# Performance work log

Measured on AMD Instinct MI355X. Metric: run time of the kernel, lower is better.

Reference implementation:

```python
import jax, jax.numpy as jnp
import numpy as np

N_NODES = 100000
N_EDGES = 1600000
N_GRAPHS = 64
D_IN = 3
HIDDEN = 256
N_CLASSES = 10
NEG_SLOPE = 0.01  # torch F.leaky_relu default


def gcn_conv(x, W, b, src, dst, n_nodes):
    """GCNConv: D^{-1/2}(A+I)D^{-1/2} X W + b with self-loops."""
    h = x @ W  # [N, H]
    ones = jnp.ones(src.shape[0], h.dtype)
    deg = jax.ops.segment_sum(ones, dst, num_segments=n_nodes) + 1.0  # +1 self-loop
    dinv = jax.lax.rsqrt(deg)
    coef = dinv[src] * dinv[dst]  # [E]
    agg = jax.ops.segment_sum(h[src] * coef[:, None], dst, num_segments=n_nodes)
    agg = agg + h * (1.0 / deg)[:, None]  # self-loop contribution (norm = 1/deg)
    return agg + b


def leaky_relu(v):
    return jnp.where(v >= 0, v, NEG_SLOPE * v)


def setup_inputs() -> dict:
    key = jax.random.key(0)
    ks = jax.random.split(key, 12)
    x = jax.random.normal(ks[0], (N_NODES, D_IN), dtype=jnp.float32)
    edge_index = jax.random.randint(ks[1], (2, N_EDGES), 0, N_NODES, dtype=jnp.int32)
    batch = jnp.sort(jax.random.randint(ks[2], (N_NODES,), 0, N_GRAPHS, dtype=jnp.int32))
    s1 = 1.0 / np.sqrt(D_IN)
    s2 = 1.0 / np.sqrt(HIDDEN)
    W1 = jax.random.uniform(ks[3], (D_IN, HIDDEN), jnp.float32, -s1, s1)
    b1 = jnp.zeros((HIDDEN,), jnp.float32)
    W2 = jax.random.uniform(ks[4], (HIDDEN, HIDDEN), jnp.float32, -s2, s2)
    b2 = jnp.zeros((HIDDEN,), jnp.float32)
    W3 = jax.random.uniform(ks[5], (HIDDEN, HIDDEN), jnp.float32, -s2, s2)
    b3 = jnp.zeros((HIDDEN,), jnp.float32)
    Wc = jax.random.uniform(ks[6], (HIDDEN, N_CLASSES), jnp.float32, -s2, s2)
    bc = jax.random.uniform(ks[7], (N_CLASSES,), jnp.float32, -s2, s2)
    return {"x": x, "edge_index": edge_index, "batch": batch,
            "W1": W1, "b1": b1, "W2": W2, "b2": b2, "W3": W3, "b3": b3,
            "Wc": Wc, "bc": bc}


def reference(x, edge_index, batch, W1, b1, W2, b2, W3, b3, Wc, bc):
    src, dst = edge_index[0], edge_index[1]
    h = leaky_relu(gcn_conv(x, W1, b1, src, dst, N_NODES))
    h = leaky_relu(gcn_conv(h, W2, b2, src, dst, N_NODES))
    h = leaky_relu(gcn_conv(h, W3, b3, src, dst, N_NODES))
    # global mean pool over graphs
    sums = jax.ops.segment_sum(h, batch, num_segments=N_GRAPHS)
    cnt = jax.ops.segment_sum(jnp.ones((N_NODES,), h.dtype), batch, num_segments=N_GRAPHS)
    pooled = sums / jnp.maximum(cnt, 1.0)[:, None]  # [G, H]
    logits = pooled @ Wc + bc
    return jax.nn.softmax(logits, axis=1)
```

## Files before the change

### kernel.cpp

```cpp
#include <hip/hip_runtime.h>
#include <hip/hip_bf16.h>
#include <hip/hip_fp16.h>
#include <cstdint>
#include <cstddef>

#define N_NODES   100000
#define N_EDGES   1600000
#define N_GRAPHS  64
#define HIDDEN    256
#define N_CLASSES 10
#define NEG_SLOPE 0.01f

#define E_PAD    (N_EDGES + 8 * N_NODES)
#define GEMM_BLOCKS 391

#define PART_EDGES  8192
#define PART_BLOCKS ((N_EDGES + PART_EDGES - 1) / PART_EDGES)
#define SUB_BITS 10
#define SUB_SIZE 1024
#define N_SUB    ((N_NODES + SUB_SIZE - 1) / SUB_SIZE)
#define CAP_SUB  17408

typedef __attribute__((ext_vector_type(4))) float f32x4;
typedef __attribute__((ext_vector_type(2))) float f32x2;

__device__ __forceinline__ float bf2f(unsigned short u) {
    return __uint_as_float(((unsigned int)u) << 16);
}

__device__ __forceinline__ unsigned char f2fp8(float v) {
    return (unsigned char)(__builtin_amdgcn_cvt_pk_fp8_f32(v, v, 0, false) & 0xff);
}

__device__ __forceinline__ unsigned int rec_pack(int s, float c) {
    __half h = __float2half(c);
    unsigned short hb = reinterpret_cast<const __half_raw*>(&h)->x;
    return ((unsigned int)hb << 17) | (unsigned int)s;
}
__device__ __forceinline__ float rec_coef(unsigned int u) {
    __half_raw hr; hr.x = (unsigned short)(u >> 17);
    return __half2float(*reinterpret_cast<const __half*>(&hr));
}

__global__ __launch_bounds__(256) void k_partition(const int* __restrict__ src, const int* __restrict__ dst,
                                                   int* __restrict__ gcur, unsigned int* __restrict__ bucket) {
    __shared__ int lcnt[N_SUB];
    __shared__ int lbase[N_SUB];
    __shared__ int gbase[N_SUB];
    __shared__ unsigned int stage[PART_EDGES];
    int tid = threadIdx.x;
    for (int i = tid; i < N_SUB; i += 256) lcnt[i] = 0;
    __syncthreads();
    int e0 = blockIdx.x * PART_EDGES + tid * 8;
    for (int g = 0; g < 4; ++g) {
        int e = e0 + g * 2048;
        if (e < N_EDGES) {
            int4 da = *(const int4*)(dst + e);
            int4 db = *(const int4*)(dst + e + 4);
            int d[8] = {da.x, da.y, da.z, da.w, db.x, db.y, db.z, db.w};
#pragma unroll
            for (int j = 0; j < 8; ++j) atomicAdd(&lcnt[d[j] >> SUB_BITS], 1);
        }
    }
    __syncthreads();
    if (tid == 0) {
        int s = 0;
        for (int r = 0; r < N_SUB; ++r) { lbase[r] = s; s += lcnt[r]; }
    }
    __syncthreads();
    for (int i = tid; i < N_SUB; i += 256) {
        gbase[i] = atomicAdd(&gcur[i * 16], lcnt[i]);
        lcnt[i] = lbase[i];
    }
    __syncthreads();
    for (int g = 0; g < 4; ++g) {
        int e = e0 + g * 2048;
        if (e < N_EDGES) {
            int4 da = *(const int4*)(dst + e);
            int4 db = *(const int4*)(dst + e + 4);
            int4 sa = *(const int4*)(src + e);
            int4 sb = *(const int4*)(src + e + 4);
            int d[8] = {da.x, da.y, da.z, da.w, db.x, db.y, db.z, db.w};
            int s[8] = {sa.x, sa.y, sa.z, sa.w, sb.x, sb.y, sb.z, sb.w};
#pragma unroll
            for (int j = 0; j < 8; ++j) {
                int r = d[j] >> SUB_BITS;
                int p = atomicAdd(&lcnt[r], 1);
                stage[p] = ((unsigned int)(d[j] & (SUB_SIZE - 1)) << 17) | (unsigned int)s[j];
            }
        }
    }
    __syncthreads();
    int wv = tid >> 6, ln = tid & 63;
    for (int r = wv; r < N_SUB; r += 4) {
        int base = lbase[r], n = lcnt[r] - base, gb = gbase[r];
        unsigned int* dp = bucket + (size_t)r * CAP_SUB + gb;
        for (int k = ln; k < n; k += 64) dp[k] = stage[base + k];
    }
}

__global__ __launch_bounds__(512) void k_hist3(const unsigned int* __restrict__ bucket,
                                               const int* __restrict__ gcur, int* __restrict__ cnt) {
    int sub = blockIdx.x;
    __shared__ int hist[SUB_SIZE];
    for (int i = threadIdx.x; i < SUB_SIZE; i += 512) hist[i] = 0;
    __syncthreads();
    int n = gcur[sub * 16];
    const unsigned int* bp = bucket + (size_t)sub * CAP_SUB;
    for (int i0 = threadIdx.x * 8; i0 < n; i0 += 512 * 8) {
        uint4 ua = *(const uint4*)(bp + i0);
        uint4 ub = *(const uint4*)(bp + i0 + 4);
        unsigned int u[8] = {ua.x, ua.y, ua.z, ua.w, ub.x, ub.y, ub.z, ub.w};
        int m = n - i0; if (m > 8) m = 8;
#pragma unroll
        for (int j = 0; j < 8; ++j) if (j < m) atomicAdd(&hist[u[j] >> 17], 1);
    }
    __syncthreads();
    int base = sub * SUB_SIZE;
    for (int i = threadIdx.x; i < SUB_SIZE; i += 512)
        if (base + i < N_NODES) cnt[base + i] = hist[i];
}

__global__ __launch_bounds__(512) void k_fill3(const unsigned int* __restrict__ bucket,
                                               const int* __restrict__ gcur,
                                               const float* __restrict__ dinv,
                                               const int* __restrict__ off,
                                               unsigned int* __restrict__ rec) {
    int sub = blockIdx.x;
    __shared__ int lcur[SUB_SIZE];
    __shared__ float ldv[SUB_SIZE];
    int nb0 = sub * SUB_SIZE;
    for (int i = threadIdx.x; i < SUB_SIZE; i += 512) {
        int node = nb0 + i;
        lcur[i] = (node < N_NODES) ? off[node] : 0;
        ldv[i]  = (node < N_NODES) ? dinv[node] : 0.f;
    }
    __syncthreads();
    int n = gcur[sub * 16];
    const unsigned int* bp = bucket + (size_t)sub * CAP_SUB;
    for (int i0 = threadIdx.x * 8; i0 < n; i0 += 512 * 8) {
        uint4 ua = *(const uint4*)(bp + i0);
        uint4 ub = *(const uint4*)(bp + i0 + 4);
        unsigned int u[8] = {ua.x, ua.y, ua.z, ua.w, ub.x, ub.y, ub.z, ub.w};
        int m = n - i0; if (m > 8) m = 8;
        float ds[8];
#pragma unroll
        for (int j = 0; j < 8; ++j) {
            int s = (j < m) ? (int)(u[j] & 0x1ffff) : 0;
            ds[j] = dinv[s];
        }
#pragma unroll
        for (int j = 0; j < 8; ++j) {
            if (j < m) {
                int dr = (int)(u[j] >> 17);
                float c = ds[j] * ldv[dr];
                int p = atomicAdd(&lcur[dr], 1);
                rec[p] = rec_pack((int)(u[j] & 0x1ffff), c);
            }
        }
    }
}

__global__ void k_graph_bounds(const int* __restrict__ batch,
                               int* __restrict__ gstart, int* __restrict__ gcnt) {
    int g = threadIdx.x;
    int lo = 0, hi = N_NODES;
    while (lo < hi) { int mid = (lo + hi) >> 1; if (batch[mid] < g) lo = mid + 1; else hi = mid; }
    __shared__ int sh[N_GRAPHS + 1];
    sh[g] = lo;
    if (g == 0) sh[N_GRAPHS] = N_NODES;
    __syncthreads();
    gstart[g] = sh[g];
    gcnt[g]   = sh[g + 1] - sh[g];
}

__global__ void k_dinv_xpad(const int* __restrict__ cnt, const float* __restrict__ x,
                            float* __restrict__ dinv, float4* __restrict__ xp) {
    int i = blockIdx.x * 256 + threadIdx.x;
    if (i < N_NODES) {
        dinv[i] = rsqrtf((float)cnt[i] + 1.0f);
        xp[i] = make_float4(x[i * 3 + 0], x[i * 3 + 1], x[i * 3 + 2], 0.f);
    }
}

__global__ void k_scanA(const int* __restrict__ cnt, int* __restrict__ out, int* __restrict__ bsum) {
    __shared__ int sh[256];
    int tid = threadIdx.x;
    int base = blockIdx.x * 1024 + tid * 4;
    int v[4]; int s = 0;
#pragma unroll
    for (int i = 0; i < 4; i++) {
        int idx = base + i;
        v[i] = (idx < N_NODES) ? ((cnt[idx] + 7) & ~7) : 0;
        s += v[i];
    }
    sh[tid] = s; __syncthreads();
    for (int off = 1; off < 256; off <<= 1) {
        int t = (tid >= off) ? sh[tid - off] : 0;
        __syncthreads();
        sh[tid] += t;
        __syncthreads();
    }
    int excl = sh[tid] - s;
    if (tid == 255) bsum[blockIdx.x] = sh[255];
#pragma unroll
    for (int i = 0; i < 4; i++) { int idx = base + i; if (idx < N_NODES) out[idx] = excl; excl += v[i]; }
}

__global__ void k_scanB(int* __restrict__ bsum, int nb) {
    __shared__ int sh[128];
    int tid = threadIdx.x;
    int v = (tid < nb) ? bsum[tid] : 0;
    sh[tid] = v; __syncthreads();
    for (int off = 1; off < 128; off <<= 1) {
        int t = (tid >= off) ? sh[tid - off] : 0;
        __syncthreads();
        sh[tid] += t;
        __syncthreads();
    }
    if (tid < nb) bsum[tid] = sh[tid] - v;
}

__global__ void k_scanC(int* __restrict__ off_arr, const int* __restrict__ bsum,
                        const int* __restrict__ cnt, unsigned int* __restrict__ rec) {
    int i = blockIdx.x * 256 + threadIdx.x;
    if (i < N_NODES) {
        int v = off_arr[i] + bsum[i >> 10];
        off_arr[i] = v;
        int c  = cnt[i];
        int cp = (c + 7) & ~7;
        for (int p = v + c; p < v + cp; ++p) rec[p] = 0u;
        if (i == N_NODES - 1) off_arr[N_NODES] = v + cp;
    }
}

__global__ void k_wprep(const float* __restrict__ W, unsigned char* __restrict__ Wswz) {
    int n = blockIdx.x; int k = threadIdx.x;
    unsigned char v = f2fp8(W[k * HIDDEN + n]);
    int k0 = k >> 5, nt = n >> 4;
    int lane = (((k >> 3) & 3) << 4) | (n & 15);
    int j = k & 7;
    Wswz[(size_t)(((k0 * 16) + nt) * 64 + lane) * 8 + j] = v;
}

__global__ void k_agg3(const float4* __restrict__ xp, const int* __restrict__ off,
                       const unsigned int* __restrict__ rec, const float* __restrict__ dinv,
                       float4* __restrict__ ax) {
    int i = blockIdx.x * 256 + threadIdx.x;
    if (i >= N_NODES) return;
    float di = dinv[i];
    float selfc = di * di;
    float4 xi = xp[i];
    float a0 = xi.x * selfc, a1 = xi.y * selfc, a2 = xi.z * selfc;
    int e = off[i], e1 = off[i + 1];
    for (; e < e1; e += 4) {
        uint4 rr = *(const uint4*)(rec + e);
        int s0 = rr.x & 0x1ffff, s1 = rr.y & 0x1ffff, s2 = rr.z & 0x1ffff, s3 = rr.w & 0x1ffff;
        float c0 = rec_coef(rr.x), c1 = rec_coef(rr.y), c2 = rec_coef(rr.z), c3 = rec_coef(rr.w);
        float4 x0 = xp[s0], x1 = xp[s1], x2 = xp[s2], x3 = xp[s3];
        a0 += c0 * x0.x + c1 * x1.x + c2 * x2.x + c3 * x3.x;
        a1 += c0 * x0.y + c1 * x1.y + c2 * x2.y + c3 * x3.y;
        a2 += c0 * x0.z + c1 * x1.z + c2 * x2.z + c3 * x3.z;
    }
    ax[i] = make_float4(a0, a1, a2, 0.f);
}

__global__ void k_l1(const float4* __restrict__ ax, const float* __restrict__ W1,
                     const float* __restrict__ b1, unsigned char* __restrict__ out) {
    int node = blockIdx.x; int c = threadIdx.x;
    float4 a = ax[node];
    float v = a.x * W1[c] + a.y * W1[HIDDEN + c] + a.z * W1[2 * HIDDEN + c] + b1[c];
    v = v >= 0.f ? v : NEG_SLOPE * v;
    out[(size_t)node * HIDDEN + c] = f2fp8(v);
}

__global__ __launch_bounds__(512, 2) void k_gemm_mfma(const unsigned char* __restrict__ A,
                                                      const unsigned char* __restrict__ Wswz,
                                                      unsigned char* __restrict__ C, int M) {
    __shared__ long Bs[8192];
    __shared__ unsigned int St[8][320];
    int tid = threadIdx.x;
    {
        const float4* gsrc = (const float4*)Wswz;
        float4* ldst = (float4*)Bs;
#pragma unroll
        for (int i = 0; i < 8; ++i) ldst[tid + 512 * i] = gsrc[tid + 512 * i];
    }
    __syncthreads();
    int lane = tid & 63, wv = tid >> 6;
    int quad = lane >> 4, r = lane & 15;
    int nstrips = M >> 4;
    unsigned int* stw = &St[wv][0];
    int rrow = lane >> 2, rseg = lane & 3;
    for (int s = blockIdx.x * 8 + wv; s < nstrips; s += GEMM_BLOCKS * 8) {
        int m0 = s * 16;
        const long* Ab = (const long*)(A + (size_t)(m0 + r) * HIDDEN) + quad;
        long af[8];
#pragma unroll
        for (int k0 = 0; k0 < 8; ++k0) af[k0] = Ab[k0 * 4];
        f32x4 acc[16];
#pragma unroll
        for (int i = 0; i < 16; i++) acc[i] = (f32x4){0.f, 0.f, 0.f, 0.f};
#pragma unroll
        for (int k0 = 0; k0 < 8; ++k0) {
#pragma unroll
            for (int nt = 0; nt < 16; ++nt) {
                long w = Bs[(k0 * 16 + nt) * 64 + lane];
                acc[nt] = __builtin_amdgcn_mfma_f32_16x16x32_fp8_fp8(w, af[k0], acc[nt], 0, 0, 0);
            }
        }
#pragma unroll
        for (int q4 = 0; q4 < 4; ++q4) {
#pragma unroll
            for (int t = 0; t < 4; ++t) {
                f32x4 a = acc[q4 * 4 + t];
                unsigned int pk = __builtin_amdgcn_cvt_pk_fp8_f32(a[0], a[1], 0, false);
                pk = __builtin_amdgcn_cvt_pk_fp8_f32(a[2], a[3], pk, true);
                stw[r * 20 + t * 4 + quad] = pk;
            }
            uint4 v = *(const uint4*)&stw[rrow * 20 + rseg * 4];
            *(uint4*)(C + (size_t)(m0 + rrow) * HIDDEN + q4 * 64 + rseg * 16) = v;
        }
    }
}

__global__ __launch_bounds__(256) void k_agg(const unsigned char* __restrict__ h,
                                             const float* __restrict__ bias,
                                             const int* __restrict__ off, const unsigned int* __restrict__ rec,
                                             const float* __restrict__ dinv,
                                             unsigned char* __restrict__ out) {
    int node = (blockIdx.x * 256 + threadIdx.x) >> 6;
    int lane = threadIdx.x & 63;
    if (node >= N_NODES) return;
    float di = dinv[node];
    float selfc = di * di;
    unsigned int hv = *(const unsigned int*)(h + (size_t)node * HIDDEN + lane * 4);
    f32x2 hlo = __builtin_amdgcn_cvt_pk_f32_fp8(hv, false);
    f32x2 hhi = __builtin_amdgcn_cvt_pk_f32_fp8(hv, true);
    float4 bv = ((const float4*)bias)[lane];
    float4 acc = make_float4(bv.x + hlo.x * selfc, bv.y + hlo.y * selfc,
                             bv.z + hhi.x * selfc, bv.w + hhi.y * selfc);
    int e = off[node], e1 = off[node + 1];
    for (; e < e1; e += 8) {
        uint4 ra = *(const uint4*)(rec + e);
        uint4 rb = *(const uint4*)(rec + e + 4);
        unsigned int w0 = *(const unsigned int*)(h + (size_t)(ra.x & 0x1ffff) * HIDDEN + lane * 4);
        unsigned int w1 = *(const unsigned int*)(h + (size_t)(ra.y & 0x1ffff) * HIDDEN + lane * 4);
        unsigned int w2 = *(const unsigned int*)(h + (size_t)(ra.z & 0x1ffff) * HIDDEN + lane * 4);
        unsigned int w3 = *(const unsigned int*)(h + (size_t)(ra.w & 0x1ffff) * HIDDEN + lane * 4);
        unsigned int w4 = *(const unsigned int*)(h + (size_t)(rb.x & 0x1ffff) * HIDDEN + lane * 4);
        unsigned int w5 = *(const unsigned int*)(h + (size_t)(rb.y & 0x1ffff) * HIDDEN + lane * 4);
        unsigned int w6 = *(const unsigned int*)(h + (size_t)(rb.z & 0x1ffff) * HIDDEN + lane * 4);
        unsigned int w7 = *(const unsigned int*)(h + (size_t)(rb.w & 0x1ffff) * HIDDEN + lane * 4);
        float c0 = rec_coef(ra.x), c1 = rec_coef(ra.y), c2 = rec_coef(ra.z), c3 = rec_coef(ra.w);
        float c4 = rec_coef(rb.x), c5 = rec_coef(rb.y), c6 = rec_coef(rb.z), c7 = rec_coef(rb.w);
        f32x2 l0 = __builtin_amdgcn_cvt_pk_f32_fp8(w0, false), g0 = __builtin_amdgcn_cvt_pk_f32_fp8(w0, true);
        f32x2 l1 = __builtin_amdgcn_cvt_pk_f32_fp8(w1, false), g1 = __builtin_amdgcn_cvt_pk_f32_fp8(w1, true);
        f32x2 l2 = __builtin_amdgcn_cvt_pk_f32_fp8(w2, false), g2 = __builtin_amdgcn_cvt_pk_f32_fp8(w2, true);
        f32x2 l3 = __builtin_amdgcn_cvt_pk_f32_fp8(w3, false), g3 = __builtin_amdgcn_cvt_pk_f32_fp8(w3, true);
        f32x2 l4 = __builtin_amdgcn_cvt_pk_f32_fp8(w4, false), g4 = __builtin_amdgcn_cvt_pk_f32_fp8(w4, true);
        f32x2 l5 = __builtin_amdgcn_cvt_pk_f32_fp8(w5, false), g5 = __builtin_amdgcn_cvt_pk_f32_fp8(w5, true);
        f32x2 l6 = __builtin_amdgcn_cvt_pk_f32_fp8(w6, false), g6 = __builtin_amdgcn_cvt_pk_f32_fp8(w6, true);
        f32x2 l7 = __builtin_amdgcn_cvt_pk_f32_fp8(w7, false), g7 = __builtin_amdgcn_cvt_pk_f32_fp8(w7, true);
        acc.x += c0 * l0.x + c1 * l1.x + c2 * l2.x + c3 * l3.x
               + c4 * l4.x + c5 * l5.x + c6 * l6.x + c7 * l7.x;
        acc.y += c0 * l0.y + c1 * l1.y + c2 * l2.y + c3 * l3.y
               + c4 * l4.y + c5 * l5.y + c6 * l6.y + c7 * l7.y;
        acc.z += c0 * g0.x + c1 * g1.x + c2 * g2.x + c3 * g3.x
               + c4 * g4.x + c5 * g5.x + c6 * g6.x + c7 * g7.x;
        acc.w += c0 * g0.y + c1 * g1.y + c2 * g2.y + c3 * g3.y
               + c4 * g4.y + c5 * g5.y + c6 * g6.y + c7 * g7.y;
    }
    acc.x = acc.x >= 0.f ? acc.x : NEG_SLOPE * acc.x;
    acc.y = acc.y >= 0.f ? acc.y : NEG_SLOPE * acc.y;
    acc.z = acc.z >= 0.f ? acc.z : NEG_SLOPE * acc.z;
    acc.w = acc.w >= 0.f ? acc.w : NEG_SLOPE * acc.w;
    unsigned int pk = __builtin_amdgcn_cvt_pk_fp8_f32(acc.x, acc.y, 0, false);
    pk = __builtin_amdgcn_cvt_pk_fp8_f32(acc.z, acc.w, pk, true);
    *(unsigned int*)(out + (size_t)node * HIDDEN + lane * 4) = pk;
}

__global__ void k_pool(const unsigned char* __restrict__ h, const int* __restrict__ gstart,
                       const int* __restrict__ gcnt, float* __restrict__ pooled) {
    int g = blockIdx.x, chunk = blockIdx.y, t = threadIdx.x;
    int s = gstart[g], c = gcnt[g];
    int i0 = s + (int)(((long long)c * chunk) / 16);
    int i1 = s + (int)(((long long)c * (chunk + 1)) / 16);
    float acc = 0.f;
    for (int i = i0; i < i1; ++i) {
        f32x2 v = __builtin_amdgcn_cvt_pk_f32_fp8((unsigned int)h[(size_t)i * HIDDEN + t], false);
        acc += v.x;
    }
    atomicAdd(&pooled[g * HIDDEN + t], acc);
}

__global__ void k_head(const float* __restrict__ pooled, const int* __restrict__ gcnt,
                       const float* __restrict__ Wc, const float* __restrict__ bc,
                       float* __restrict__ out) {
    int g = blockIdx.x; int l = threadIdx.x;
    float inv = 1.0f / fmaxf((float)gcnt[g], 1.0f);
    float p[4];
#pragma unroll
    for (int i = 0; i < 4; i++) p[i] = pooled[g * HIDDEN + l + i * 64] * inv;
    __shared__ float logits[N_CLASSES];
#pragma unroll
    for (int j = 0; j < N_CLASSES; j++) {
        float s = 0.f;
#pragma unroll
        for (int i = 0; i < 4; i++) s += p[i] * Wc[(l + i * 64) * N_CLASSES + j];
        for (int o = 32; o > 0; o >>= 1) s += __shfl_down(s, o, 64);
        if (l == 0) logits[j] = s + bc[j];
    }
    __syncthreads();
    if (l == 0) {
        float m = logits[0];
        for (int j = 1; j < N_CLASSES; j++) m = fmaxf(m, logits[j]);
        float e[N_CLASSES]; float sum = 0.f;
        for (int j = 0; j < N_CLASSES; j++) { e[j] = expf(logits[j] - m); sum += e[j]; }
        for (int j = 0; j < N_CLASSES; j++) out[g * N_CLASSES + j] = e[j] / sum;
    }
}

extern "C" void kernel_launch(void* const* d_in, const int* in_sizes, int n_in,
                              void* d_out, int out_size, void* d_ws, size_t ws_size,
                              hipStream_t stream) {
    const float* x     = (const float*)d_in[0];
    const int*   edge  = (const int*)d_in[1];
    const int*   batch = (const int*)d_in[2];
    const float* W1 = (const float*)d_in[3];
    const float* b1 = (const float*)d_in[4];
    const float* W2 = (const float*)d_in[5];
    const float* b2 = (const float*)d_in[6];
    const float* W3 = (const float*)d_in[7];
    const float* b3 = (const float*)d_in[8];
    const float* Wc = (const float*)d_in[9];
    const float* bc = (const float*)d_in[10];
    float* out = (float*)d_out;
    const int* srcp = edge;
    const int* dstp = edge + N_EDGES;

    char* ws = (char*)d_ws;
    size_t off = 0;
    auto alloc = [&](size_t bytes) -> char* {
        char* p = ws + off;
        off += (bytes + 255) & ~(size_t)255;
        return p;
    };
    unsigned char* hA   = (unsigned char*)alloc((size_t)N_NODES * HIDDEN);
    unsigned char* hB   = (unsigned char*)alloc((size_t)N_NODES * HIDDEN);
    unsigned char* Wz2  = (unsigned char*)alloc((size_t)HIDDEN * HIDDEN);
    unsigned char* Wz3  = (unsigned char*)alloc((size_t)HIDDEN * HIDDEN);
    int*   deg_cnt  = (int*)alloc((size_t)N_NODES * 4);
    float* dinv     = (float*)alloc((size_t)N_NODES * 4);
    int*   csr_off  = (int*)alloc((size_t)(N_NODES + 1) * 4);
    unsigned int* csr_rec = (unsigned int*)alloc((size_t)E_PAD * 4);
    float4* ax      = (float4*)alloc((size_t)N_NODES * 16);
    float4* xp      = (float4*)alloc((size_t)N_NODES * 16);
    int*   gcnt     = (int*)alloc((size_t)N_GRAPHS * 4);
    int*   gstart   = (int*)alloc((size_t)N_GRAPHS * 4);
    float* pooled   = (float*)alloc((size_t)N_GRAPHS * HIDDEN * 4);
    int*   bsum     = (int*)alloc(128 * 4);
    int*   gcur     = (int*)alloc((size_t)N_SUB * 16 * 4);

    unsigned int* bucket = (unsigned int*)hB;

    hipMemsetAsync(gcur, 0, (size_t)N_SUB * 16 * 4, stream);
    hipMemsetAsync(pooled, 0, (size_t)N_GRAPHS * HIDDEN * 4, stream);

    int nb  = (N_NODES + 255) / 256;
    int sblocks = (N_NODES + 1023) / 1024;

    k_partition<<<PART_BLOCKS, 256, 0, stream>>>(srcp, dstp, gcur, bucket);
    k_graph_bounds<<<1, 64, 0, stream>>>(batch, gstart, gcnt);
    k_hist3<<<N_SUB, 512, 0, stream>>>(bucket, gcur, deg_cnt);
    k_dinv_xpad<<<nb, 256, 0, stream>>>(deg_cnt, x, dinv, xp);
    k_scanA<<<sblocks, 256, 0, stream>>>(deg_cnt, csr_off, bsum);
    k_scanB<<<1, 128, 0, stream>>>(bsum, sblocks);
    k_scanC<<<nb, 256, 0, stream>>>(csr_off, bsum, deg_cnt, csr_rec);
    k_fill3<<<N_SUB, 512, 0, stream>>>(bucket, gcur, dinv, csr_off, csr_rec);
    k_wprep<<<HIDDEN, HIDDEN, 0, stream>>>(W2, Wz2);
    k_wprep<<<HIDDEN, HIDDEN, 0, stream>>>(W3, Wz3);

    k_agg3<<<nb, 256, 0, stream>>>(xp, csr_off, csr_rec, dinv, ax);
    k_l1<<<N_NODES, 256, 0, stream>>>(ax, W1, b1, hA);

    int aggb = (N_NODES + 3) / 4;
    k_gemm_mfma<<<GEMM_BLOCKS, 512, 0, stream>>>(hA, Wz2, hB, N_NODES);
    k_agg<<<aggb, 256, 0, stream>>>(hB, b2, csr_off, csr_rec, dinv, hA);
    k_gemm_mfma<<<GEMM_BLOCKS, 512, 0, stream>>>(hA, Wz3, hB, N_NODES);
    k_agg<<<aggb, 256, 0, stream>>>(hB, b3, csr_off, csr_rec, dinv, hA);
    dim3 pg(N_GRAPHS, 16);
    k_pool<<<pg, 256, 0, stream>>>(hA, gstart, gcnt, pooled);
    k_head<<<N_GRAPHS, 64, 0, stream>>>(pooled, gcnt, Wc, bc, out);
}
```

Measured before the change: 455.7 us.

## Fuse dinv/xpad into hist, batch layer-1 nodes per block, column-slice aggregation

Folds the dinv and padded-x computation into the degree histogram kernel, which removes one launch and one re-read of the counts. Layer-1 projection now handles 32 nodes per block with W1 and b1 cached in shared memory, instead of one block per node. The aggregation kernel now assigns 8 threads per node, each covering a 32-column slice, and spreads the 8 slices across consecutive blocks. The intent is to cut per-node gather traffic per block and improve cache locality, at the cost of re-reading the CSR records 8 times.

After: 702.1 us. 54.1% more time.

```diff
diff --git a/kernel.cpp b/kernel.cpp
--- a/kernel.cpp
+++ b/kernel.cpp
@@ -100,7 +100,9 @@
 }
 
 __global__ __launch_bounds__(512) void k_hist3(const unsigned int* __restrict__ bucket,
-                                               const int* __restrict__ gcur, int* __restrict__ cnt) {
+                                               const int* __restrict__ gcur, int* __restrict__ cnt,
+                                               const float* __restrict__ x,
+                                               float* __restrict__ dinv, float4* __restrict__ xp) {
     int sub = blockIdx.x;
     __shared__ int hist[SUB_SIZE];
     for (int i = threadIdx.x; i < SUB_SIZE; i += 512) hist[i] = 0;
@@ -117,8 +119,15 @@
     }
     __syncthreads();
     int base = sub * SUB_SIZE;
-    for (int i = threadIdx.x; i < SUB_SIZE; i += 512)
-        if (base + i < N_NODES) cnt[base + i] = hist[i];
+    for (int i = threadIdx.x; i < SUB_SIZE; i += 512) {
+        int node = base + i;
+        if (node < N_NODES) {
+            int c = hist[i];
+            cnt[node] = c;
+            dinv[node] = rsqrtf((float)c + 1.0f);
+            xp[node] = make_float4(x[node * 3 + 0], x[node * 3 + 1], x[node * 3 + 2], 0.f);
+        }
+    }
 }
 
 __global__ __launch_bounds__(512) void k_fill3(const unsigned int* __restrict__ bucket,
@@ -172,15 +181,6 @@
     __syncthreads();
     gstart[g] = sh[g];
     gcnt[g]   = sh[g + 1] - sh[g];
-}
-
-__global__ void k_dinv_xpad(const int* __restrict__ cnt, const float* __restrict__ x,
-                            float* __restrict__ dinv, float4* __restrict__ xp) {
-    int i = blockIdx.x * 256 + threadIdx.x;
-    if (i < N_NODES) {
-        dinv[i] = rsqrtf((float)cnt[i] + 1.0f);
-        xp[i] = make_float4(x[i * 3 + 0], x[i * 3 + 1], x[i * 3 + 2], 0.f);
-    }
 }
 
 __global__ void k_scanA(const int* __restrict__ cnt, int* __restrict__ out, int* __restrict__ bsum) {
@@ -265,13 +265,22 @@
     ax[i] = make_float4(a0, a1, a2, 0.f);
 }
 
-__global__ void k_l1(const float4* __restrict__ ax, const float* __restrict__ W1,
-                     const float* __restrict__ b1, unsigned char* __restrict__ out) {
-    int node = blockIdx.x; int c = threadIdx.x;
-    float4 a = ax[node];
-    float v = a.x * W1[c] + a.y * W1[HIDDEN + c] + a.z * W1[2 * HIDDEN + c] + b1[c];
-    v = v >= 0.f ? v : NEG_SLOPE * v;
-    out[(size_t)node * HIDDEN + c] = f2fp8(v);
+__global__ __launch_bounds__(256) void k_l1(const float4* __restrict__ ax, const float* __restrict__ W1,
+                                            const float* __restrict__ b1, unsigned char* __restrict__ out) {
+    __shared__ float w0s[HIDDEN], w1s[HIDDEN], w2s[HIDDEN], bbs[HIDDEN];
+    int t = threadIdx.x;
+    w0s[t] = W1[t]; w1s[t] = W1[HIDDEN + t]; w2s[t] = W1[2 * HIDDEN + t]; bbs[t] = b1[t];
+    __syncthreads();
+    int base = blockIdx.x * 32;
+#pragma unroll 4
+    for (int i = 0; i < 32; ++i) {
+        int node = base + i;
+        if (node >= N_NODES) break;
+        float4 a = ax[node];
+        float v = a.x * w0s[t] + a.y * w1s[t] + a.z * w2s[t] + bbs[t];
+        v = v >= 0.f ? v : NEG_SLOPE * v;
+        out[(size_t)node * HIDDEN + t] = f2fp8(v);
+    }
 }
 
 __global__ __launch_bounds__(512, 2) void k_gemm_mfma(const unsigned char* __restrict__ A,
@@ -329,29 +338,31 @@
                                              const int* __restrict__ off, const unsigned int* __restrict__ rec,
                                              const float* __restrict__ dinv,
                                              unsigned char* __restrict__ out) {
-    int node = (blockIdx.x * 256 + threadIdx.x) >> 6;
-    int lane = threadIdx.x & 63;
+    int slice = blockIdx.x & 7;
+    int node = (blockIdx.x >> 3) * 32 + (threadIdx.x >> 3);
+    int sl = threadIdx.x & 7;
     if (node >= N_NODES) return;
+    int coloff = slice * 32 + sl * 4;
     float di = dinv[node];
     float selfc = di * di;
-    unsigned int hv = *(const unsigned int*)(h + (size_t)node * HIDDEN + lane * 4);
+    unsigned int hv = *(const unsigned int*)(h + (size_t)node * HIDDEN + coloff);
     f32x2 hlo = __builtin_amdgcn_cvt_pk_f32_fp8(hv, false);
     f32x2 hhi = __builtin_amdgcn_cvt_pk_f32_fp8(hv, true);
-    float4 bv = ((const float4*)bias)[lane];
-    float4 acc = make_float4(bv.x + hlo.x * selfc, bv.y + hlo.y * selfc,
-                             bv.z + hhi.x * selfc, bv.w + hhi.y * selfc);
+    float4 bv = *(const float4*)(bias + coloff);
+    float a0 = bv.x + hlo.x * selfc, a1 = bv.y + hlo.y * selfc;
+    float a2 = bv.z + hhi.x * selfc, a3 = bv.w + hhi.y * selfc;
     int e = off[node], e1 = off[node + 1];
     for (; e < e1; e += 8) {
         uint4 ra = *(const uint4*)(rec + e);
         uint4 rb = *(const uint4*)(rec + e + 4);
-        unsigned int w0 = *(const unsigned int*)(h + (size_t)(ra.x & 0x1ffff) * HIDDEN + lane * 4);
-        unsigned int w1 = *(const unsigned int*)(h + (size_t)(ra.y & 0x1ffff) * HIDDEN + lane * 4);
-        unsigned int w2 = *(const unsigned int*)(h + (size_t)(ra.z & 0x1ffff) * HIDDEN + lane * 4);
-        unsigned int w3 = *(const unsigned int*)(h + (size_t)(ra.w & 0x1ffff) * HIDDEN + lane * 4);
-        unsigned int w4 = *(const unsigned int*)(h + (size_t)(rb.x & 0x1ffff) * HIDDEN + lane * 4);
-        unsigned int w5 = *(const unsigned int*)(h + (size_t)(rb.y & 0x1ffff) * HIDDEN + lane * 4);
-        unsigned int w6 = *(const unsigned int*)(h + (size_t)(rb.z & 0x1ffff) * HIDDEN + lane * 4);
-        unsigned int w7 = *(const unsigned int*)(h + (size_t)(rb.w & 0x1ffff) * HIDDEN + lane * 4);
+        unsigned int w0 = *(const unsigned int*)(h + (size_t)(ra.x & 0x1ffff) * HIDDEN + coloff);
+        unsigned int w1 = *(const unsigned int*)(h + (size_t)(ra.y & 0x1ffff) * HIDDEN + coloff);
+        unsigned int w2 = *(const unsigned int*)(h + (size_t)(ra.z & 0x1ffff) * HIDDEN + coloff);
+        unsigned int w3 = *(const unsigned int*)(h + (size_t)(ra.w & 0x1ffff) * HIDDEN + coloff);
+        unsigned int w4 = *(const unsigned int*)(h + (size_t)(rb.x & 0x1ffff) * HIDDEN + coloff);
+        unsigned int w5 = *(const unsigned int*)(h + (size_t)(rb.y & 0x1ffff) * HIDDEN + coloff);
+        unsigned int w6 = *(const unsigned int*)(h + (size_t)(rb.z & 0x1ffff) * HIDDEN + coloff);
+        unsigned int w7 = *(const unsigned int*)(h + (size_t)(rb.w & 0x1ffff) * HIDDEN + coloff);
         float c0 = rec_coef(ra.x), c1 = rec_coef(ra.y), c2 = rec_coef(ra.z), c3 = rec_coef(ra.w);
         float c4 = rec_coef(rb.x), c5 = rec_coef(rb.y), c6 = rec_coef(rb.z), c7 = rec_coef(rb.w);
         f32x2 l0 = __builtin_amdgcn_cvt_pk_f32_fp8(w0, false), g0 = __builtin_amdgcn_cvt_pk_f32_fp8(w0, true);
@@ -362,22 +373,22 @@
         f32x2 l5 = __builtin_amdgcn_cvt_pk_f32_fp8(w5, false), g5 = __builtin_amdgcn_cvt_pk_f32_fp8(w5, true);
         f32x2 l6 = __builtin_amdgcn_cvt_pk_f32_fp8(w6, false), g6 = __builtin_amdgcn_cvt_pk_f32_fp8(w6, true);
         f32x2 l7 = __builtin_amdgcn_cvt_pk_f32_fp8(w7, false), g7 = __builtin_amdgcn_cvt_pk_f32_fp8(w7, true);
-        acc.x += c0 * l0.x + c1 * l1.x + c2 * l2.x + c3 * l3.x
-               + c4 * l4.x + c5 * l5.x + c6 * l6.x + c7 * l7.x;
-        acc.y += c0 * l0.y + c1 * l1.y + c2 * l2.y + c3 * l3.y
-               + c4 * l4.y + c5 * l5.y + c6 * l6.y + c7 * l7.y;
-        acc.z += c0 * g0.x + c1 * g1.x + c2 * g2.x + c3 * g3.x
-               + c4 * g4.x + c5 * g5.x + c6 * g6.x + c7 * g7.x;
-        acc.w += c0 * g0.y + c1 * g1.y + c2 * g2.y + c3 * g3.y
-               + c4 * g4.y + c5 * g5.y + c6 * g6.y + c7 * g7.y;
-    }
-    acc.x = acc.x >= 0.f ? acc.x : NEG_SLOPE * acc.x;
-    acc.y = acc.y >= 0.f ? acc.y : NEG_SLOPE * acc.y;
-    acc.z = acc.z >= 0.f ? acc.z : NEG_SLOPE * acc.z;
-    acc.w = acc.w >= 0.f ? acc.w : NEG_SLOPE * acc.w;
-    unsigned int pk = __builtin_amdgcn_cvt_pk_fp8_f32(acc.x, acc.y, 0, false);
-    pk = __builtin_amdgcn_cvt_pk_fp8_f32(acc.z, acc.w, pk, true);
-    *(unsigned int*)(out + (size_t)node * HIDDEN + lane * 4) = pk;
+        a0 += c0 * l0.x + c1 * l1.x + c2 * l2.x + c3 * l3.x
+            + c4 * l4.x + c5 * l5.x + c6 * l6.x + c7 * l7.x;
+        a1 += c0 * l0.y + c1 * l1.y + c2 * l2.y + c3 * l3.y
+            + c4 * l4.y + c5 * l5.y + c6 * l6.y + c7 * l7.y;
+        a2 += c0 * g0.x + c1 * g1.x + c2 * g2.x + c3 * g3.x
+            + c4 * g4.x + c5 * g5.x + c6 * g6.x + c7 * g7.x;
+        a3 += c0 * g0.y + c1 * g1.y + c2 * g2.y + c3 * g3.y
+            + c4 * g4.y + c5 * g5.y + c6 * g6.y + c7 * g7.y;
+    }
+    a0 = a0 >= 0.f ? a0 : NEG_SLOPE * a0;
+    a1 = a1 >= 0.f ? a1 : NEG_SLOPE * a1;
+    a2 = a2 >= 0.f ? a2 : NEG_SLOPE * a2;
+    a3 = a3 >= 0.f ? a3 : NEG_SLOPE * a3;
+    unsigned int pk = __builtin_amdgcn_cvt_pk_fp8_f32(a0, a1, 0, false);
+    pk = __builtin_amdgcn_cvt_pk_fp8_f32(a2, a3, pk, true);
+    *(unsigned int*)(out + (size_t)node * HIDDEN + coloff) = pk;
 }
 
 __global__ void k_pool(const unsigned char* __restrict__ h, const int* __restrict__ gstart,
@@ -472,8 +483,7 @@
 
     k_partition<<<PART_BLOCKS, 256, 0, stream>>>(srcp, dstp, gcur, bucket);
     k_graph_bounds<<<1, 64, 0, stream>>>(batch, gstart, gcnt);
-    k_hist3<<<N_SUB, 512, 0, stream>>>(bucket, gcur, deg_cnt);
-    k_dinv_xpad<<<nb, 256, 0, stream>>>(deg_cnt, x, dinv, xp);
+    k_hist3<<<N_SUB, 512, 0, stream>>>(bucket, gcur, deg_cnt, x, dinv, xp);
     k_scanA<<<sblocks, 256, 0, stream>>>(deg_cnt, csr_off, bsum);
     k_scanB<<<1, 128, 0, stream>>>(bsum, sblocks);
     k_scanC<<<nb, 256, 0, stream>>>(csr_off, bsum, deg_cnt, csr_rec);
@@ -482,9 +492,9 @@
     k_wprep<<<HIDDEN, HIDDEN, 0, stream>>>(W3, Wz3);
 
     k_agg3<<<nb, 256, 0, stream>>>(xp, csr_off, csr_rec, dinv, ax);
-    k_l1<<<N_NODES, 256, 0, stream>>>(ax, W1, b1, hA);
-
-    int aggb = (N_NODES + 3) / 4;
+    k_l1<<<(N_NODES + 31) / 32, 256, 0, stream>>>(ax, W1, b1, hA);
+
+    int aggb = ((N_NODES + 31) / 32) * 8;
     k_gemm_mfma<<<GEMM_BLOCKS, 512, 0, stream>>>(hA, Wz2, hB, N_NODES);
     k_agg<<<aggb, 256, 0, stream>>>(hB, b2, csr_off, csr_rec, dinv, hA);
     k_gemm_mfma<<<GEMM_BLOCKS, 512, 0, stream>>>(hA, Wz3, hB, N_NODES);
```
